# Optimization experiments

Hardware: AMD Instinct MI355X
Metric: run time of the kernel (lower is better)

Reference implementation:

```python
import jax, jax.numpy as jnp
import numpy as np

B, S, IN1, IN2, H = 1024, 200, 128, 128, 128

def setup_inputs() -> dict:
    key = jax.random.key(0)
    k = jax.random.split(key, 8)
    inp = jax.random.normal(k[0], (B, S, IN1), dtype=jnp.float32)
    z = jax.random.normal(k[1], (B, IN2), dtype=jnp.float32)
    mask = jax.random.randint(k[2], (B, S), 0, 2, dtype=jnp.int32)
    # learned params (PyTorch Linear: y = x @ W.T + b; store transposed for x @ W)
    W1 = jax.random.normal(k[3], (IN1, H), dtype=jnp.float32) / np.sqrt(IN1)
    W2 = jax.random.normal(k[4], (IN2, H), dtype=jnp.float32) / np.sqrt(IN2)
    b2 = jax.random.normal(k[5], (H,), dtype=jnp.float32) * 0.02
    V = jax.random.normal(k[6], (H, 1), dtype=jnp.float32) / np.sqrt(H)
    bV = jax.random.normal(k[7], (1,), dtype=jnp.float32) * 0.02
    return {"input": inp, "z": z, "mask": mask, "W1": W1, "W2": W2, "b2": b2, "V": V, "bV": bV}

def reference(input, z, mask, W1, W2, b2, V, bV):
    # w1h: [B,S,H]; w2h: [B,1,H]
    w1h = jnp.einsum('bsd,dh->bsh', input, W1)
    w2h = (z @ W2 + b2)[:, None, :]
    u = jnp.tanh(w1h + w2h)                      # [B,S,H]
    att = (jnp.einsum('bsh,h->bs', u, V[:, 0]) + bV[0])  # [B,S]
    att = jnp.where(mask == 0, jnp.float32(-1e10), att)
    att = jax.nn.softmax(att, axis=1)            # softmax over S
    out = jnp.einsum('bs,bsd->bd', att, input)   # weighted sum pooling
    return out
```

## Files before the change

kernel.cpp:

```cpp
#include <hip/hip_runtime.h>
#include <hip/hip_bf16.h>

constexpr int S_ = 200;
constexpr int SP = 208;

typedef __attribute__((ext_vector_type(8))) short short8_t;
typedef __attribute__((ext_vector_type(4))) float float4_t;

__device__ inline unsigned short f2bf(float f) {
  unsigned int u = __float_as_uint(f);
  u += 0x7FFFu + ((u >> 16) & 1u);
  return (unsigned short)(u >> 16);
}
__device__ inline unsigned int pk2(float x, float y) {
  return (unsigned int)f2bf(x) | ((unsigned int)f2bf(y) << 16);
}

__global__ __launch_bounds__(256, 4) void m2o_attn_kernel(
    const float* __restrict__ input, const float* __restrict__ z,
    const int* __restrict__ mask, const float* __restrict__ W1,
    const float* __restrict__ W2, const float* __restrict__ b2,
    const float* __restrict__ V, const float* __restrict__ bV,
    float* __restrict__ out) {
  __shared__ float w2h_part[2][128];
  __shared__ float att_part[2][SP];
  __shared__ float att_w[SP];
  __shared__ float pool[2][128];
  __shared__ float redA[4], redB[4];

  const int t = threadIdx.x;
  const int b = blockIdx.x;
  const int lane = t & 63;
  const int wid = t >> 6;
  const int c = lane & 15;
  const int kb = lane >> 4;

  const float* inb = input + (size_t)b * (S_ * 128);

  const int maskv = (t < S_) ? mask[(size_t)b * S_ + t] : 0;
  const float bVv = bV[0];

  {
    const int h = t & 127, ph = t >> 7;
    const float* zb = z + (size_t)b * 128 + ph * 64;
    float acc = (ph == 0) ? b2[h] : 0.f;
    #pragma unroll 8
    for (int d = 0; d < 64; ++d) acc = fmaf(zb[d], W2[(ph * 64 + d) * 128 + h], acc);
    w2h_part[ph][h] = acc;
  }

  const int hh = (wid & 1) * 64;
  short8_t bfrag[4][4];
  #pragma unroll
  for (int n = 0; n < 4; ++n) {
    const int h = hh + n * 16 + c;
    #pragma unroll
    for (int kk = 0; kk < 4; ++kk) {
      union { short8_t s8; unsigned int u[4]; } cv;
      #pragma unroll
      for (int jp = 0; jp < 4; ++jp) {
        const int k = kk * 32 + kb * 8 + jp * 2;
        cv.u[jp] = pk2(W1[k * 128 + h], W1[(k + 1) * 128 + h]);
      }
      bfrag[n][kk] = cv.s8;
    }
  }
  float vv[4];
  #pragma unroll
  for (int n = 0; n < 4; ++n) vv[n] = V[hh + n * 16 + c];

  __syncthreads();

  float w2v[4];
  #pragma unroll
  for (int n = 0; n < 4; ++n) {
    const int h = hh + n * 16 + c;
    w2v[n] = w2h_part[0][h] + w2h_part[1][h];
  }

  const int half = wid >> 1;
  const int pslot = wid & 1;
  const int mt0 = half * 7;
  const int nmt = half ? 6 : 7;

  float4 pa[4][2];
  {
    const int arow = mt0 * 16 + c;
    const int lrow = arow < S_ ? arow : (S_ - 1);
    const float* rp = inb + lrow * 128 + kb * 8;
    #pragma unroll
    for (int kk = 0; kk < 4; ++kk) {
      pa[kk][0] = *reinterpret_cast<const float4*>(rp + kk * 32);
      pa[kk][1] = *reinterpret_cast<const float4*>(rp + kk * 32 + 4);
    }
  }

  for (int i = 0; i < nmt; ++i) {
    const int mt = mt0 + i;
    short8_t a[4];
    #pragma unroll
    for (int kk = 0; kk < 4; ++kk) {
      union { short8_t s8; unsigned int u[4]; } cv;
      cv.u[0] = pk2(pa[kk][0].x, pa[kk][0].y);
      cv.u[1] = pk2(pa[kk][0].z, pa[kk][0].w);
      cv.u[2] = pk2(pa[kk][1].x, pa[kk][1].y);
      cv.u[3] = pk2(pa[kk][1].z, pa[kk][1].w);
      a[kk] = cv.s8;
    }
    if (i + 1 < nmt) {
      const int arow = (mt + 1) * 16 + c;
      const int lrow = arow < S_ ? arow : (S_ - 1);
      const float* rp = inb + lrow * 128 + kb * 8;
      #pragma unroll
      for (int kk = 0; kk < 4; ++kk) {
        pa[kk][0] = *reinterpret_cast<const float4*>(rp + kk * 32);
        pa[kk][1] = *reinterpret_cast<const float4*>(rp + kk * 32 + 4);
      }
    }
    float4_t acc[4] = {{0.f, 0.f, 0.f, 0.f}, {0.f, 0.f, 0.f, 0.f},
                       {0.f, 0.f, 0.f, 0.f}, {0.f, 0.f, 0.f, 0.f}};
    #pragma unroll
    for (int kk = 0; kk < 4; ++kk) {
      #pragma unroll
      for (int n = 0; n < 4; ++n)
        acc[n] = __builtin_amdgcn_mfma_f32_16x16x32_bf16(a[kk], bfrag[n][kk], acc[n], 0, 0, 0);
    }
    #pragma unroll
    for (int r = 0; r < 4; ++r) {
      const int row = mt * 16 + kb * 4 + r;
      float p = 0.f;
      #pragma unroll
      for (int n = 0; n < 4; ++n) {
        const float x = acc[n][r] + w2v[n];
        const float e = __expf(x + x);
        const float u = 1.f - __fdividef(2.f, e + 1.f);
        p = fmaf(u, vv[n], p);
      }
      p += __shfl_xor(p, 1);
      p += __shfl_xor(p, 2);
      p += __shfl_xor(p, 4);
      p += __shfl_xor(p, 8);
      if (c == 0 && row < S_) att_part[pslot][row] = p;
    }
  }
  __syncthreads();

  float logit = -3.0e38f, ee = 0.f;
  if (t < S_) {
    logit = att_part[0][t] + att_part[1][t] + bVv;
    if (maskv == 0) logit = -1e10f;
  }
  {
    float m = logit;
    #pragma unroll
    for (int off = 32; off; off >>= 1) m = fmaxf(m, __shfl_xor(m, off));
    if (lane == 0) redA[wid] = m;
  }
  __syncthreads();
  {
    const float M = fmaxf(fmaxf(redA[0], redA[1]), fmaxf(redA[2], redA[3]));
    ee = (t < S_) ? __expf(logit - M) : 0.f;
    float sg = ee;
    #pragma unroll
    for (int off = 32; off; off >>= 1) sg += __shfl_xor(sg, off);
    if (lane == 0) redB[wid] = sg;
  }
  __syncthreads();
  {
    const float Ssum = redB[0] + redB[1] + redB[2] + redB[3];
    if (t < SP) att_w[t] = (t < S_) ? __fdividef(ee, Ssum) : 0.f;
  }
  __syncthreads();

  {
    const int d = t & 127, ph = t >> 7;
    const float* pp = inb + (size_t)(ph * 100) * 128 + d;
    float a0 = 0.f;
    #pragma unroll 4
    for (int s = 0; s < 100; ++s) a0 = fmaf(att_w[ph * 100 + s], pp[s * 128], a0);
    pool[ph][d] = a0;
  }
  __syncthreads();
  if (t < 128) out[(size_t)b * 128 + t] = pool[0][t] + pool[1][t];
}

extern "C" void kernel_launch(void* const* d_in, const int* in_sizes, int n_in,
                              void* d_out, int out_size, void* d_ws, size_t ws_size,
                              hipStream_t stream) {
  const float* input = (const float*)d_in[0];
  const float* z     = (const float*)d_in[1];
  const int*   mask  = (const int*)d_in[2];
  const float* W1    = (const float*)d_in[3];
  const float* W2    = (const float*)d_in[4];
  const float* b2    = (const float*)d_in[5];
  const float* V     = (const float*)d_in[6];
  const float* bV    = (const float*)d_in[7];
  float* out = (float*)d_out;
  m2o_attn_kernel<<<1024, 256, 0, stream>>>(input, z, mask, W1, W2, b2, V, bV, out);
}
```

Baseline: 196.2 us.

## Precompute bf16 W1 MFMA fragments in a prep kernel and stage in LDS

```diff
diff --git a/kernel.cpp b/kernel.cpp
--- a/kernel.cpp
+++ b/kernel.cpp
@@ -16,12 +16,28 @@
   return (unsigned int)f2bf(x) | ((unsigned int)f2bf(y) << 16);
 }
 
+__global__ __launch_bounds__(256) void prep_frag_kernel(
+    const float* __restrict__ W1, short8_t* __restrict__ frag_out) {
+  const int fid = blockIdx.x * 256 + threadIdx.x;
+  const int lane = fid & 63, kk = (fid >> 6) & 3, nh = fid >> 8;
+  const int c = lane & 15, kb = lane >> 4;
+  const int h = nh * 16 + c;
+  union { short8_t s8; unsigned int u[4]; } cv;
+  #pragma unroll
+  for (int jp = 0; jp < 4; ++jp) {
+    const int k = kk * 32 + kb * 8 + jp * 2;
+    cv.u[jp] = pk2(W1[k * 128 + h], W1[(k + 1) * 128 + h]);
+  }
+  frag_out[fid] = cv.s8;
+}
+
 __global__ __launch_bounds__(256, 4) void m2o_attn_kernel(
     const float* __restrict__ input, const float* __restrict__ z,
-    const int* __restrict__ mask, const float* __restrict__ W1,
-    const float* __restrict__ W2, const float* __restrict__ b2,
-    const float* __restrict__ V, const float* __restrict__ bV,
+    const int* __restrict__ mask, const float* __restrict__ W2,
+    const float* __restrict__ b2, const float* __restrict__ V,
+    const float* __restrict__ bV, const short8_t* __restrict__ frag,
     float* __restrict__ out) {
+  __shared__ short8_t frag_lds[2048];
   __shared__ float w2h_part[2][128];
   __shared__ float att_part[2][SP];
   __shared__ float att_w[SP];
@@ -37,6 +53,9 @@
 
   const float* inb = input + (size_t)b * (S_ * 128);
 
+  #pragma unroll
+  for (int i = 0; i < 8; ++i) frag_lds[t + i * 256] = frag[t + i * 256];
+
   const int maskv = (t < S_) ? mask[(size_t)b * S_ + t] : 0;
   const float bVv = bV[0];
 
@@ -49,22 +68,7 @@
     w2h_part[ph][h] = acc;
   }
 
-  const int hh = (wid & 1) * 64;
-  short8_t bfrag[4][4];
-  #pragma unroll
-  for (int n = 0; n < 4; ++n) {
-    const int h = hh + n * 16 + c;
-    #pragma unroll
-    for (int kk = 0; kk < 4; ++kk) {
-      union { short8_t s8; unsigned int u[4]; } cv;
-      #pragma unroll
-      for (int jp = 0; jp < 4; ++jp) {
-        const int k = kk * 32 + kb * 8 + jp * 2;
-        cv.u[jp] = pk2(W1[k * 128 + h], W1[(k + 1) * 128 + h]);
-      }
-      bfrag[n][kk] = cv.s8;
-    }
-  }
+  const int hh_i = wid & 1, hh = hh_i * 64;
   float vv[4];
   #pragma unroll
   for (int n = 0; n < 4; ++n) vv[n] = V[hh + n * 16 + c];
@@ -79,7 +83,6 @@
   }
 
   const int half = wid >> 1;
-  const int pslot = wid & 1;
   const int mt0 = half * 7;
   const int nmt = half ? 6 : 7;
 
@@ -123,7 +126,8 @@
     for (int kk = 0; kk < 4; ++kk) {
       #pragma unroll
       for (int n = 0; n < 4; ++n)
-        acc[n] = __builtin_amdgcn_mfma_f32_16x16x32_bf16(a[kk], bfrag[n][kk], acc[n], 0, 0, 0);
+        acc[n] = __builtin_amdgcn_mfma_f32_16x16x32_bf16(
+            a[kk], frag_lds[((hh_i * 4 + n) * 4 + kk) * 64 + lane], acc[n], 0, 0, 0);
     }
     #pragma unroll
     for (int r = 0; r < 4; ++r) {
@@ -140,7 +144,7 @@
       p += __shfl_xor(p, 2);
       p += __shfl_xor(p, 4);
       p += __shfl_xor(p, 8);
-      if (c == 0 && row < S_) att_part[pslot][row] = p;
+      if (c == 0 && row < S_) att_part[hh_i][row] = p;
     }
   }
   __syncthreads();
@@ -196,5 +200,9 @@
   const float* V     = (const float*)d_in[6];
   const float* bV    = (const float*)d_in[7];
   float* out = (float*)d_out;
-  m2o_attn_kernel<<<1024, 256, 0, stream>>>(input, z, mask, W1, W2, b2, V, bV, out);
-}
+
+  short8_t* frag_ws = (short8_t*)d_ws;
+  prep_frag_kernel<<<8, 256, 0, stream>>>(W1, frag_ws);
+  m2o_attn_kernel<<<1024, 256, 0, stream>>>(input, z, mask, W2, b2, V, bV,
+                                            frag_ws, out);
+}
```

Measured after the change: 196.9 us. Within noise of the previous version (+0.4%).
